# Kernel optimization log

Measured on AMD Instinct MI355X. Metric: run time of the kernel, lower is better.

Reference implementation:

```python
import jax, jax.numpy as jnp
import numpy as np

B = 16384       # batch
G = 8           # groups
S = 16          # state_c (per-group in/out channels)
H = 512         # hidden_c (per-group hidden channels)
FACTOR = 1.0
SWISH_DIV = 1.1


def setup_inputs() -> dict:
    key = jax.random.key(0)
    ks = jax.random.split(key, 12)
    def w(k, shape, fan_in):
        bound = 1.0 / np.sqrt(fan_in)
        return jax.random.uniform(k, shape, jnp.float32, -bound, bound)
    return {
        "x":  jax.random.normal(ks[0], (B, G * S), dtype=jnp.float32),
        # grouped 1x1 convs as per-group linear weights [G, out_c, in_c]
        "W1": w(ks[1], (G, H, S), S), "b1": w(ks[2], (G, H), S),
        "beta1": jnp.full((G,), 0.5, jnp.float32),
        "W2": w(ks[3], (G, H, H), H), "b2": w(ks[4], (G, H), H),
        "beta2": jnp.full((G,), 0.5, jnp.float32),
        "W3": w(ks[5], (G, H, H), H), "b3": w(ks[6], (G, H), H),
        "beta3": jnp.full((G,), 0.5, jnp.float32),
        "W4": w(ks[7], (G, S, H), H), "b4": w(ks[8], (G, S), H),
    }


def _group_swish(x, beta):
    # x: [B, G, C]; beta: [G] -> y = x * sigmoid(x * softplus(beta)) / 1.1
    sp = jax.nn.softplus(beta)[None, :, None]
    return x * jax.nn.sigmoid(x * sp) / SWISH_DIV


def reference(x, W1, b1, beta1, W2, b2, beta2, W3, b3, beta3, W4, b4):
    h = x.reshape(-1, G, S)                                   # [B,G,S]
    h = jnp.einsum('bgs,ghs->bgh', h, W1) + b1[None]          # [B,G,H]
    h = _group_swish(h, beta1)
    h = jnp.einsum('bgi,goi->bgo', h, W2) + b2[None]
    h = _group_swish(h, beta2)
    h = jnp.einsum('bgi,goi->bgo', h, W3) + b3[None]
    h = _group_swish(h, beta3)
    h = jnp.einsum('bgh,gsh->bgs', h, W4) + b4[None]          # [B,G,S]
    return h.reshape(-1, G * S) * FACTOR
```

## Files before the change

kernel.cpp:

```cpp
#include <hip/hip_runtime.h>
#include <stdint.h>

#define G_ 8
#define S_ 16
#define H_ 512
#define TB 64
#define NTH 512

typedef _Float16 h16;
typedef _Float16 h16x8 __attribute__((ext_vector_type(8)));
typedef float f32x4 __attribute__((ext_vector_type(4)));
typedef float f32x16 __attribute__((ext_vector_type(16)));

#define HB_BYTES (TB * 1024)
#define XB_BYTES 2048
#define SMEM_BYTES (HB_BYTES + XB_BYTES)


__device__ __forceinline__ float swishf(float v, float sp) {
    const float e = __expf(-v * sp);
    return v * __builtin_amdgcn_rcpf(1.0f + e) * (1.0f / 1.1f);
}

__device__ __forceinline__ uint32_t pk16(float a, float b) {
    return __builtin_bit_cast(uint32_t, __builtin_amdgcn_cvt_pkrtz(a, b));
}

template<bool USEWS>
__device__ __forceinline__ h16x8 loadA32ks(const h16* __restrict__ wpk,
                                           const float* __restrict__ wf,
                                           int ks, int nb, int ln, int Ksrc) {
    if constexpr (USEWS) {
        return *(const h16x8*)(wpk + (((size_t)ks * 16 + nb) * 64 + ln) * 8);
    } else {
        const int row = nb * 32 + (ln & 31);
        const int k = ks * 16 + (ln >> 5) * 8;
        const float* p = wf + (size_t)row * Ksrc + k;
        h16x8 r;
        #pragma unroll
        for (int j = 0; j < 8; ++j) r[j] = (h16)p[j];
        return r;
    }
}

template<bool USEWS>
__device__ __forceinline__ h16x8 loadA16(const h16* __restrict__ wpk,
                                         const float* __restrict__ wf,
                                         int ks32, int ln, int Ksrc) {
    if constexpr (USEWS) {
        return *(const h16x8*)(wpk + ((size_t)ks32 * 64 + ln) * 8);
    } else {
        const int row = ln & 15;
        const int k = ks32 * 32 + (ln >> 4) * 8;
        const float* p = wf + (size_t)row * Ksrc + k;
        h16x8 r;
        #pragma unroll
        for (int j = 0; j < 8; ++j) r[j] = (h16)p[j];
        return r;
    }
}

__device__ __forceinline__ void swish_store32(const f32x16 (&acc)[2][2], char* hb,
                                              const float* __restrict__ bias, float sp,
                                              int wv, int ln) {
    const int l31 = ln & 31, lh = ln >> 5;
    char* const wbase = hb + wv * 8192 + l31 * 16 + lh * 8;
    #pragma unroll
    for (int ot = 0; ot < 2; ++ot) {
        #pragma unroll
        for (int rq = 0; rq < 4; ++rq) {
            const int col0 = wv * 64 + ot * 32 + rq * 8 + lh * 4;
            const f32x4 bv = *(const f32x4*)(bias + col0);
            #pragma unroll
            for (int bt = 0; bt < 2; ++bt) {
                const float v0 = swishf(acc[ot][bt][rq * 4 + 0] + bv[0], sp);
                const float v1 = swishf(acc[ot][bt][rq * 4 + 1] + bv[1], sp);
                const float v2 = swishf(acc[ot][bt][rq * 4 + 2] + bv[2], sp);
                const float v3 = swishf(acc[ot][bt][rq * 4 + 3] + bv[3], sp);
                const uint64_t u = (uint64_t)pk16(v0, v1)
                                 | ((uint64_t)pk16(v2, v3) << 32);
                *(uint64_t*)(wbase + (ot * 4 + rq) * 1024 + bt * 512) = u;
            }
        }
    }
}

template<bool USEWS>
__device__ __forceinline__ void layerH32(f32x16 (&acc)[2][2],
                                         const h16* __restrict__ wpk, const float* __restrict__ wf,
                                         const char* __restrict__ hb, int wv, int ln) {
    const int l31 = ln & 31, lh = ln >> 5;
    const char* const bbase = hb + l31 * 16 + lh * 1024;
    const int nb0 = wv * 2;
    #pragma unroll
    for (int ot = 0; ot < 2; ++ot)
        #pragma unroll
        for (int bt = 0; bt < 2; ++bt) acc[ot][bt] = (f32x16)(0.f);

    h16x8 aC0 = loadA32ks<USEWS>(wpk, wf, 0, nb0 + 0, ln, H_);
    h16x8 aC1 = loadA32ks<USEWS>(wpk, wf, 0, nb0 + 1, ln, H_);

    #pragma unroll 4
    for (int ks = 0; ks < 32; ++ks) {
        const int ksn = (ks + 1 < 32) ? ks + 1 : 0;
        h16x8 aN0 = loadA32ks<USEWS>(wpk, wf, ksn, nb0 + 0, ln, H_);
        h16x8 aN1 = loadA32ks<USEWS>(wpk, wf, ksn, nb0 + 1, ln, H_);
        const h16x8 b0 = *(const h16x8*)(bbase + ks * 2048);
        const h16x8 b1 = *(const h16x8*)(bbase + ks * 2048 + 512);
        __builtin_amdgcn_s_setprio(1);
        acc[0][0] = __builtin_amdgcn_mfma_f32_32x32x16_f16(aC0, b0, acc[0][0], 0, 0, 0);
        acc[0][1] = __builtin_amdgcn_mfma_f32_32x32x16_f16(aC0, b1, acc[0][1], 0, 0, 0);
        acc[1][0] = __builtin_amdgcn_mfma_f32_32x32x16_f16(aC1, b0, acc[1][0], 0, 0, 0);
        acc[1][1] = __builtin_amdgcn_mfma_f32_32x32x16_f16(aC1, b1, acc[1][1], 0, 0, 0);
        __builtin_amdgcn_s_setprio(0);
        aC0 = aN0; aC1 = aN1;
    }
}

template<bool USEWS>
__global__ __launch_bounds__(NTH, 4) void mlp_fused(
    const float* __restrict__ x,
    const float* __restrict__ W1f, const float* __restrict__ b1, const float* __restrict__ be1,
    const float* __restrict__ W2f, const float* __restrict__ b2, const float* __restrict__ be2,
    const float* __restrict__ W3f, const float* __restrict__ b3, const float* __restrict__ be3,
    const float* __restrict__ W4f, const float* __restrict__ b4,
    const h16* __restrict__ W1p, const h16* __restrict__ W2p,
    const h16* __restrict__ W3p, const h16* __restrict__ W4p,
    float* __restrict__ out) {
    extern __shared__ char smem[];
    char* __restrict__ xb = smem + HB_BYTES;

    const int bid = blockIdx.x;
    const int g = bid & 7;
    const int rowbase = (bid >> 3) * TB;
    const int tid = threadIdx.x;
    const int wv = tid >> 6;
    const int ln = tid & 63;
    const int l31 = ln & 31;
    const int lh = ln >> 5;

    const float sp1 = log1pf(__expf(be1[g]));
    const float sp2 = log1pf(__expf(be2[g]));
    const float sp3 = log1pf(__expf(be3[g]));

    const h16* w1p = W1p + (size_t)g * H_ * S_;
    const h16* w2p = W2p + (size_t)g * H_ * H_;
    const h16* w3p = W3p + (size_t)g * H_ * H_;
    const h16* w4p = W4p + (size_t)g * S_ * H_;
    const float* w1f = W1f + (size_t)g * H_ * S_;
    const float* w2f = W2f + (size_t)g * H_ * H_;
    const float* w3f = W3f + (size_t)g * H_ * H_;
    const float* w4f = W4f + (size_t)g * S_ * H_;

    {
        const int idx = tid * 2;
        const int r = idx >> 4, s = idx & 15;
        const float2 v = *(const float2*)(x + (size_t)(rowbase + r) * (G_ * S_) + g * S_ + s);
        *(uint32_t*)(xb + (s >> 3) * 1024 + r * 16 + (s & 7) * 2) = pk16(v.x, v.y);
    }
    __syncthreads();

    f32x16 acc[2][2];

    {
        #pragma unroll
        for (int ot = 0; ot < 2; ++ot)
            #pragma unroll
            for (int bt = 0; bt < 2; ++bt) acc[ot][bt] = (f32x16)(0.f);
        const char* const xbase = xb + l31 * 16 + lh * 1024;
        h16x8 aW[2], bX[2];
        #pragma unroll
        for (int ot = 0; ot < 2; ++ot)
            aW[ot] = loadA32ks<USEWS>(w1p, w1f, 0, wv * 2 + ot, ln, S_);
        #pragma unroll
        for (int bt = 0; bt < 2; ++bt)
            bX[bt] = *(const h16x8*)(xbase + bt * 512);
        #pragma unroll
        for (int ot = 0; ot < 2; ++ot)
            #pragma unroll
            for (int bt = 0; bt < 2; ++bt)
                acc[ot][bt] = __builtin_amdgcn_mfma_f32_32x32x16_f16(aW[ot], bX[bt],
                                                                     acc[ot][bt], 0, 0, 0);
    }
    swish_store32(acc, smem, b1 + g * H_, sp1, wv, ln);
    __syncthreads();

    layerH32<USEWS>(acc, w2p, w2f, smem, wv, ln);
    __syncthreads();
    swish_store32(acc, smem, b2 + g * H_, sp2, wv, ln);
    __syncthreads();

    layerH32<USEWS>(acc, w3p, w3f, smem, wv, ln);
    __syncthreads();
    swish_store32(acc, smem, b3 + g * H_, sp3, wv, ln);
    __syncthreads();

    if (wv < 4) {
        f32x4 a4 = {0.f, 0.f, 0.f, 0.f};
        const int l15 = ln & 15, lq = ln >> 4;
        const char* const b4base = smem + lq * 1024 + (wv * 16 + l15) * 16;
        #pragma unroll 4
        for (int ks = 0; ks < 16; ++ks) {
            const h16x8 a = loadA16<USEWS>(w4p, w4f, ks, ln, H_);
            const h16x8 b = *(const h16x8*)(b4base + ks * 4096);
            a4 = __builtin_amdgcn_mfma_f32_16x16x32_f16(a, b, a4, 0, 0, 0);
        }
        const int brow = wv * 16 + l15;
        const int s0 = lq * 4;
        const f32x4 bv = *(const f32x4*)(b4 + g * S_ + s0);
        f32x4 o4;
        #pragma unroll
        for (int r = 0; r < 4; ++r) o4[r] = a4[r] + bv[r];
        *(f32x4*)(out + (size_t)(rowbase + brow) * (G_ * S_) + g * S_ + s0) = o4;
    }
}

__global__ void packW32(const float* __restrict__ s, h16* __restrict__ d,
                        int KB, int Ks) {
    const int t = blockIdx.x * 256 + threadIdx.x;
    const int total = G_ * KB * 16 * 64;
    if (t >= total) return;
    const int ln = t & 63;
    const int blk = t >> 6;
    const int nb = blk & 15;
    const int rest = blk >> 4;
    const int ks = rest % KB;
    const int g = rest / KB;
    const int row = g * H_ + nb * 32 + (ln & 31);
    const int k = ks * 16 + (ln >> 5) * 8;
    const float* p = s + (size_t)row * Ks + k;
    h16x8 o;
    #pragma unroll
    for (int j = 0; j < 8; ++j) o[j] = (h16)p[j];
    *(h16x8*)(d + (size_t)t * 8) = o;
}

__global__ void packW16(const float* __restrict__ s, h16* __restrict__ d,
                        int NB_total, int KB, int Ks) {
    const int t = blockIdx.x * 256 + threadIdx.x;
    const int total = NB_total * KB * 64;
    if (t >= total) return;
    const int ln = t & 63;
    const int blk = t >> 6;
    const int kb = blk % KB;
    const int nbg = blk / KB;
    const int row = nbg * 16 + (ln & 15);
    const int k = kb * 32 + (ln >> 4) * 8;
    const float* p = s + (size_t)row * Ks + k;
    h16x8 o;
    #pragma unroll
    for (int j = 0; j < 8; ++j) o[j] = (h16)p[j];
    *(h16x8*)(d + (size_t)t * 8) = o;
}

extern "C" void kernel_launch(void* const* d_in, const int* in_sizes, int n_in,
                              void* d_out, int out_size, void* d_ws, size_t ws_size,
                              hipStream_t stream) {
    const float* x   = (const float*)d_in[0];
    const float* W1  = (const float*)d_in[1];
    const float* b1  = (const float*)d_in[2];
    const float* be1 = (const float*)d_in[3];
    const float* W2  = (const float*)d_in[4];
    const float* b2  = (const float*)d_in[5];
    const float* be2 = (const float*)d_in[6];
    const float* W3  = (const float*)d_in[7];
    const float* b3  = (const float*)d_in[8];
    const float* be3 = (const float*)d_in[9];
    const float* W4  = (const float*)d_in[10];
    const float* b4  = (const float*)d_in[11];
    float* out = (float*)d_out;

    const size_t nW2  = (size_t)G_ * H_ * H_;
    const size_t nW1p = (size_t)G_ * H_ * S_;
    const size_t nW4  = (size_t)G_ * S_ * H_;
    const size_t need = (2 * nW2 + nW1p + nW4) * sizeof(h16);

    const dim3 grid(2048), blk(NTH);

    if (ws_size >= need) {
        h16* W2p = (h16*)d_ws;
        h16* W3p = W2p + nW2;
        h16* W1p = W3p + nW2;
        h16* W4p = W1p + nW1p;
        packW32<<<dim3((unsigned)((nW2 / 8 + 255) / 256)), dim3(256), 0, stream>>>(W2, W2p, 32, H_);
        packW32<<<dim3((unsigned)((nW2 / 8 + 255) / 256)), dim3(256), 0, stream>>>(W3, W3p, 32, H_);
        packW32<<<dim3((unsigned)((nW1p / 8 + 255) / 256)), dim3(256), 0, stream>>>(W1, W1p, 1, S_);
        packW16<<<dim3((unsigned)((nW4 / 8 + 255) / 256)), dim3(256), 0, stream>>>(W4, W4p, G_, 16, H_);
        (void)hipFuncSetAttribute(reinterpret_cast<const void*>(mlp_fused<true>),
                                  hipFuncAttributeMaxDynamicSharedMemorySize, (int)SMEM_BYTES);
        mlp_fused<true><<<grid, blk, SMEM_BYTES, stream>>>(
            x, W1, b1, be1, W2, b2, be2, W3, b3, be3, W4, b4,
            W1p, W2p, W3p, W4p, out);
    } else {
        (void)hipFuncSetAttribute(reinterpret_cast<const void*>(mlp_fused<false>),
                                  hipFuncAttributeMaxDynamicSharedMemorySize, (int)SMEM_BYTES);
        mlp_fused<false><<<grid, blk, SMEM_BYTES, stream>>>(
            x, W1, b1, be1, W2, b2, be2, W3, b3, be3, W4, b4,
            nullptr, nullptr, nullptr, nullptr, out);
    }
}
```

Before: 198.2 us.

## Double batch tile to 128 rows with 16 waves splitting output and batch halves

Doubles the per-block batch tile to 128 rows and the block to 1024 threads. Wave pairs share an output slice and each covers one half of the batch, so every weight fragment loaded from global memory serves twice as many rows, halving weight traffic per row. The shared-memory layout for activations is restrided to fit 128 rows, and the grid is halved. It also drops the software prefetch of the next A fragment in the hidden-layer loop, which may expose global load latency, and the larger blocks with __launch_bounds__(1024,4) add register pressure and lower block-level occupancy.

```diff
diff --git a/kernel.cpp b/kernel.cpp
--- a/kernel.cpp
+++ b/kernel.cpp
@@ -4,8 +4,8 @@
 #define G_ 8
 #define S_ 16
 #define H_ 512
-#define TB 64
-#define NTH 512
+#define TB 128
+#define NTH 1024
 
 typedef _Float16 h16;
 typedef _Float16 h16x8 __attribute__((ext_vector_type(8)));
@@ -13,7 +13,7 @@
 typedef float f32x16 __attribute__((ext_vector_type(16)));
 
 #define HB_BYTES (TB * 1024)
-#define XB_BYTES 2048
+#define XB_BYTES (TB * 32)
 #define SMEM_BYTES (HB_BYTES + XB_BYTES)
 
 
@@ -62,14 +62,14 @@
 
 __device__ __forceinline__ void swish_store32(const f32x16 (&acc)[2][2], char* hb,
                                               const float* __restrict__ bias, float sp,
-                                              int wv, int ln) {
+                                              int os, int bh, int ln) {
     const int l31 = ln & 31, lh = ln >> 5;
-    char* const wbase = hb + wv * 8192 + l31 * 16 + lh * 8;
+    char* const wbase = hb + os * 16384 + bh * 1024 + l31 * 16 + lh * 8;
     #pragma unroll
     for (int ot = 0; ot < 2; ++ot) {
         #pragma unroll
         for (int rq = 0; rq < 4; ++rq) {
-            const int col0 = wv * 64 + ot * 32 + rq * 8 + lh * 4;
+            const int col0 = os * 64 + ot * 32 + rq * 8 + lh * 4;
             const f32x4 bv = *(const f32x4*)(bias + col0);
             #pragma unroll
             for (int bt = 0; bt < 2; ++bt) {
@@ -79,7 +79,7 @@
                 const float v3 = swishf(acc[ot][bt][rq * 4 + 3] + bv[3], sp);
                 const uint64_t u = (uint64_t)pk16(v0, v1)
                                  | ((uint64_t)pk16(v2, v3) << 32);
-                *(uint64_t*)(wbase + (ot * 4 + rq) * 1024 + bt * 512) = u;
+                *(uint64_t*)(wbase + (ot * 4 + rq) * 2048 + bt * 512) = u;
             }
         }
     }
@@ -88,32 +88,27 @@
 template<bool USEWS>
 __device__ __forceinline__ void layerH32(f32x16 (&acc)[2][2],
                                          const h16* __restrict__ wpk, const float* __restrict__ wf,
-                                         const char* __restrict__ hb, int wv, int ln) {
+                                         const char* __restrict__ hb, int os, int bh, int ln) {
     const int l31 = ln & 31, lh = ln >> 5;
-    const char* const bbase = hb + l31 * 16 + lh * 1024;
-    const int nb0 = wv * 2;
+    const char* const bbase = hb + lh * 2048 + bh * 1024 + l31 * 16;
+    const int nb0 = os * 2;
     #pragma unroll
     for (int ot = 0; ot < 2; ++ot)
         #pragma unroll
         for (int bt = 0; bt < 2; ++bt) acc[ot][bt] = (f32x16)(0.f);
-
-    h16x8 aC0 = loadA32ks<USEWS>(wpk, wf, 0, nb0 + 0, ln, H_);
-    h16x8 aC1 = loadA32ks<USEWS>(wpk, wf, 0, nb0 + 1, ln, H_);
 
     #pragma unroll 4
     for (int ks = 0; ks < 32; ++ks) {
-        const int ksn = (ks + 1 < 32) ? ks + 1 : 0;
-        h16x8 aN0 = loadA32ks<USEWS>(wpk, wf, ksn, nb0 + 0, ln, H_);
-        h16x8 aN1 = loadA32ks<USEWS>(wpk, wf, ksn, nb0 + 1, ln, H_);
-        const h16x8 b0 = *(const h16x8*)(bbase + ks * 2048);
-        const h16x8 b1 = *(const h16x8*)(bbase + ks * 2048 + 512);
+        const h16x8 a0 = loadA32ks<USEWS>(wpk, wf, ks, nb0 + 0, ln, H_);
+        const h16x8 a1 = loadA32ks<USEWS>(wpk, wf, ks, nb0 + 1, ln, H_);
+        const h16x8 b0 = *(const h16x8*)(bbase + ks * 4096);
+        const h16x8 b1 = *(const h16x8*)(bbase + ks * 4096 + 512);
         __builtin_amdgcn_s_setprio(1);
-        acc[0][0] = __builtin_amdgcn_mfma_f32_32x32x16_f16(aC0, b0, acc[0][0], 0, 0, 0);
-        acc[0][1] = __builtin_amdgcn_mfma_f32_32x32x16_f16(aC0, b1, acc[0][1], 0, 0, 0);
-        acc[1][0] = __builtin_amdgcn_mfma_f32_32x32x16_f16(aC1, b0, acc[1][0], 0, 0, 0);
-        acc[1][1] = __builtin_amdgcn_mfma_f32_32x32x16_f16(aC1, b1, acc[1][1], 0, 0, 0);
+        acc[0][0] = __builtin_amdgcn_mfma_f32_32x32x16_f16(a0, b0, acc[0][0], 0, 0, 0);
+        acc[0][1] = __builtin_amdgcn_mfma_f32_32x32x16_f16(a0, b1, acc[0][1], 0, 0, 0);
+        acc[1][0] = __builtin_amdgcn_mfma_f32_32x32x16_f16(a1, b0, acc[1][0], 0, 0, 0);
+        acc[1][1] = __builtin_amdgcn_mfma_f32_32x32x16_f16(a1, b1, acc[1][1], 0, 0, 0);
         __builtin_amdgcn_s_setprio(0);
-        aC0 = aN0; aC1 = aN1;
     }
 }
 
@@ -138,6 +133,8 @@
     const int ln = tid & 63;
     const int l31 = ln & 31;
     const int lh = ln >> 5;
+    const int os = wv >> 1;
+    const int bh = wv & 1;
 
     const float sp1 = log1pf(__expf(be1[g]));
     const float sp2 = log1pf(__expf(be2[g]));
@@ -156,7 +153,7 @@
         const int idx = tid * 2;
         const int r = idx >> 4, s = idx & 15;
         const float2 v = *(const float2*)(x + (size_t)(rowbase + r) * (G_ * S_) + g * S_ + s);
-        *(uint32_t*)(xb + (s >> 3) * 1024 + r * 16 + (s & 7) * 2) = pk16(v.x, v.y);
+        *(uint32_t*)(xb + (s >> 3) * 2048 + r * 16 + (s & 7) * 2) = pk16(v.x, v.y);
     }
     __syncthreads();
 
@@ -167,11 +164,11 @@
         for (int ot = 0; ot < 2; ++ot)
             #pragma unroll
             for (int bt = 0; bt < 2; ++bt) acc[ot][bt] = (f32x16)(0.f);
-        const char* const xbase = xb + l31 * 16 + lh * 1024;
+        const char* const xbase = xb + lh * 2048 + bh * 1024 + l31 * 16;
         h16x8 aW[2], bX[2];
         #pragma unroll
         for (int ot = 0; ot < 2; ++ot)
-            aW[ot] = loadA32ks<USEWS>(w1p, w1f, 0, wv * 2 + ot, ln, S_);
+            aW[ot] = loadA32ks<USEWS>(w1p, w1f, 0, os * 2 + ot, ln, S_);
         #pragma unroll
         for (int bt = 0; bt < 2; ++bt)
             bX[bt] = *(const h16x8*)(xbase + bt * 512);
@@ -182,27 +179,27 @@
                 acc[ot][bt] = __builtin_amdgcn_mfma_f32_32x32x16_f16(aW[ot], bX[bt],
                                                                      acc[ot][bt], 0, 0, 0);
     }
-    swish_store32(acc, smem, b1 + g * H_, sp1, wv, ln);
-    __syncthreads();
-
-    layerH32<USEWS>(acc, w2p, w2f, smem, wv, ln);
-    __syncthreads();
-    swish_store32(acc, smem, b2 + g * H_, sp2, wv, ln);
-    __syncthreads();
-
-    layerH32<USEWS>(acc, w3p, w3f, smem, wv, ln);
-    __syncthreads();
-    swish_store32(acc, smem, b3 + g * H_, sp3, wv, ln);
-    __syncthreads();
-
-    if (wv < 4) {
+    swish_store32(acc, smem, b1 + g * H_, sp1, os, bh, ln);
+    __syncthreads();
+
+    layerH32<USEWS>(acc, w2p, w2f, smem, os, bh, ln);
+    __syncthreads();
+    swish_store32(acc, smem, b2 + g * H_, sp2, os, bh, ln);
+    __syncthreads();
+
+    layerH32<USEWS>(acc, w3p, w3f, smem, os, bh, ln);
+    __syncthreads();
+    swish_store32(acc, smem, b3 + g * H_, sp3, os, bh, ln);
+    __syncthreads();
+
+    if (wv < 8) {
         f32x4 a4 = {0.f, 0.f, 0.f, 0.f};
         const int l15 = ln & 15, lq = ln >> 4;
-        const char* const b4base = smem + lq * 1024 + (wv * 16 + l15) * 16;
+        const char* const b4base = smem + lq * 2048 + (wv * 16 + l15) * 16;
         #pragma unroll 4
         for (int ks = 0; ks < 16; ++ks) {
             const h16x8 a = loadA16<USEWS>(w4p, w4f, ks, ln, H_);
-            const h16x8 b = *(const h16x8*)(b4base + ks * 4096);
+            const h16x8 b = *(const h16x8*)(b4base + ks * 8192);
             a4 = __builtin_amdgcn_mfma_f32_16x16x32_f16(a, b, a4, 0, 0, 0);
         }
         const int brow = wv * 16 + l15;
@@ -275,7 +272,7 @@
     const size_t nW4  = (size_t)G_ * S_ * H_;
     const size_t need = (2 * nW2 + nW1p + nW4) * sizeof(h16);
 
-    const dim3 grid(2048), blk(NTH);
+    const dim3 grid((16384 / TB) * G_), blk(NTH);
 
     if (ws_size >= need) {
         h16* W2p = (h16*)d_ws;
```

Measured after the change: 213.4 us. 1.08x slower.

## Replace block barriers with per-wave LDS flags for layer handoff

Applied to the files above, without the earlier changes.

Drops the __syncthreads between the hidden layers and uses per-wave done and read counters in shared memory. Each wave spins until the slice of activations it needs has been written, and waits for all readers to finish before overwriting its own slice. The K loop is reordered so each wave starts on its own slice and rotates through the others, letting waves overlap across layers instead of waiting at a barrier. This adds spin-wait cost, drops the software prefetch of A across iterations, and risks memory-ordering bugs since the fences are only compiler and lgkmcnt waits.

```diff
diff --git a/kernel.cpp b/kernel.cpp
--- a/kernel.cpp
+++ b/kernel.cpp
@@ -14,8 +14,18 @@
 
 #define HB_BYTES (TB * 1024)
 #define XB_BYTES 2048
-#define SMEM_BYTES (HB_BYTES + XB_BYTES)
-
+#define FLAG_BYTES 128
+#define SMEM_BYTES (HB_BYTES + XB_BYTES + FLAG_BYTES)
+
+
+__device__ __forceinline__ void fence_acquire() {
+    __builtin_amdgcn_sched_barrier(0);
+    asm volatile("" ::: "memory");
+}
+__device__ __forceinline__ void fence_release() {
+    asm volatile("s_waitcnt lgkmcnt(0)" ::: "memory");
+    __builtin_amdgcn_sched_barrier(0);
+}
 
 __device__ __forceinline__ float swishf(float v, float sp) {
     const float e = __expf(-v * sp);
@@ -60,9 +70,16 @@
     }
 }
 
+template<bool FLAGS>
 __device__ __forceinline__ void swish_store32(const f32x16 (&acc)[2][2], char* hb,
                                               const float* __restrict__ bias, float sp,
-                                              int wv, int ln) {
+                                              int wv, int ln,
+                                              int* rdone, volatile int* wdone,
+                                              int need, int wseq) {
+    if constexpr (FLAGS) {
+        while (*(volatile int*)&rdone[wv] < need) { }
+        fence_acquire();
+    }
     const int l31 = ln & 31, lh = ln >> 5;
     char* const wbase = hb + wv * 8192 + l31 * 16 + lh * 8;
     #pragma unroll
@@ -83,12 +100,17 @@
             }
         }
     }
-}
-
-template<bool USEWS>
+    if constexpr (FLAGS) {
+        fence_release();
+        if (ln == 0) *(volatile int*)&wdone[wv] = wseq;
+    }
+}
+
+template<bool USEWS, bool POLLW>
 __device__ __forceinline__ void layerH32(f32x16 (&acc)[2][2],
                                          const h16* __restrict__ wpk, const float* __restrict__ wf,
-                                         const char* __restrict__ hb, int wv, int ln) {
+                                         const char* __restrict__ hb, int wv, int ln,
+                                         volatile int* wdone, int* rdone, int wseq) {
     const int l31 = ln & 31, lh = ln >> 5;
     const char* const bbase = hb + l31 * 16 + lh * 1024;
     const int nb0 = wv * 2;
@@ -97,23 +119,29 @@
         #pragma unroll
         for (int bt = 0; bt < 2; ++bt) acc[ot][bt] = (f32x16)(0.f);
 
-    h16x8 aC0 = loadA32ks<USEWS>(wpk, wf, 0, nb0 + 0, ln, H_);
-    h16x8 aC1 = loadA32ks<USEWS>(wpk, wf, 0, nb0 + 1, ln, H_);
-
-    #pragma unroll 4
-    for (int ks = 0; ks < 32; ++ks) {
-        const int ksn = (ks + 1 < 32) ? ks + 1 : 0;
-        h16x8 aN0 = loadA32ks<USEWS>(wpk, wf, ksn, nb0 + 0, ln, H_);
-        h16x8 aN1 = loadA32ks<USEWS>(wpk, wf, ksn, nb0 + 1, ln, H_);
-        const h16x8 b0 = *(const h16x8*)(bbase + ks * 2048);
-        const h16x8 b1 = *(const h16x8*)(bbase + ks * 2048 + 512);
-        __builtin_amdgcn_s_setprio(1);
-        acc[0][0] = __builtin_amdgcn_mfma_f32_32x32x16_f16(aC0, b0, acc[0][0], 0, 0, 0);
-        acc[0][1] = __builtin_amdgcn_mfma_f32_32x32x16_f16(aC0, b1, acc[0][1], 0, 0, 0);
-        acc[1][0] = __builtin_amdgcn_mfma_f32_32x32x16_f16(aC1, b0, acc[1][0], 0, 0, 0);
-        acc[1][1] = __builtin_amdgcn_mfma_f32_32x32x16_f16(aC1, b1, acc[1][1], 0, 0, 0);
-        __builtin_amdgcn_s_setprio(0);
-        aC0 = aN0; aC1 = aN1;
+    for (int i = 0; i < 8; ++i) {
+        const int q = (wv + i) & 7;
+        if constexpr (POLLW) {
+            while (wdone[q] < wseq) { }
+            fence_acquire();
+        }
+        const char* const qb = bbase + q * 8192;
+        #pragma unroll 2
+        for (int j = 0; j < 4; ++j) {
+            const int ks = q * 4 + j;
+            const h16x8 a0 = loadA32ks<USEWS>(wpk, wf, ks, nb0 + 0, ln, H_);
+            const h16x8 a1 = loadA32ks<USEWS>(wpk, wf, ks, nb0 + 1, ln, H_);
+            const h16x8 b0 = *(const h16x8*)(qb + j * 2048);
+            const h16x8 b1 = *(const h16x8*)(qb + j * 2048 + 512);
+            __builtin_amdgcn_s_setprio(1);
+            acc[0][0] = __builtin_amdgcn_mfma_f32_32x32x16_f16(a0, b0, acc[0][0], 0, 0, 0);
+            acc[0][1] = __builtin_amdgcn_mfma_f32_32x32x16_f16(a0, b1, acc[0][1], 0, 0, 0);
+            acc[1][0] = __builtin_amdgcn_mfma_f32_32x32x16_f16(a1, b0, acc[1][0], 0, 0, 0);
+            acc[1][1] = __builtin_amdgcn_mfma_f32_32x32x16_f16(a1, b1, acc[1][1], 0, 0, 0);
+            __builtin_amdgcn_s_setprio(0);
+        }
+        fence_release();
+        if (ln == 0) atomicAdd(&rdone[q], 1);
     }
 }
 
@@ -129,6 +157,9 @@
     float* __restrict__ out) {
     extern __shared__ char smem[];
     char* __restrict__ xb = smem + HB_BYTES;
+    int* const flagbase = (int*)(smem + HB_BYTES + XB_BYTES);
+    volatile int* const wdone = (volatile int*)flagbase;
+    int* const rdone = flagbase + 8;
 
     const int bid = blockIdx.x;
     const int g = bid & 7;
@@ -152,6 +183,7 @@
     const float* w3f = W3f + (size_t)g * H_ * H_;
     const float* w4f = W4f + (size_t)g * S_ * H_;
 
+    if (tid < 16) flagbase[tid] = 0;
     {
         const int idx = tid * 2;
         const int r = idx >> 4, s = idx & 15;
@@ -182,28 +214,30 @@
                 acc[ot][bt] = __builtin_amdgcn_mfma_f32_32x32x16_f16(aW[ot], bX[bt],
                                                                      acc[ot][bt], 0, 0, 0);
     }
-    swish_store32(acc, smem, b1 + g * H_, sp1, wv, ln);
+    swish_store32<false>(acc, smem, b1 + g * H_, sp1, wv, ln, nullptr, nullptr, 0, 0);
     __syncthreads();
 
-    layerH32<USEWS>(acc, w2p, w2f, smem, wv, ln);
-    __syncthreads();
-    swish_store32(acc, smem, b2 + g * H_, sp2, wv, ln);
-    __syncthreads();
-
-    layerH32<USEWS>(acc, w3p, w3f, smem, wv, ln);
-    __syncthreads();
-    swish_store32(acc, smem, b3 + g * H_, sp3, wv, ln);
-    __syncthreads();
+    layerH32<USEWS, false>(acc, w2p, w2f, smem, wv, ln, wdone, rdone, 0);
+    swish_store32<true>(acc, smem, b2 + g * H_, sp2, wv, ln, rdone, wdone, 8, 2);
+
+    layerH32<USEWS, true>(acc, w3p, w3f, smem, wv, ln, wdone, rdone, 2);
+    swish_store32<true>(acc, smem, b3 + g * H_, sp3, wv, ln, rdone, wdone, 16, 3);
 
     if (wv < 4) {
         f32x4 a4 = {0.f, 0.f, 0.f, 0.f};
         const int l15 = ln & 15, lq = ln >> 4;
         const char* const b4base = smem + lq * 1024 + (wv * 16 + l15) * 16;
-        #pragma unroll 4
-        for (int ks = 0; ks < 16; ++ks) {
-            const h16x8 a = loadA16<USEWS>(w4p, w4f, ks, ln, H_);
-            const h16x8 b = *(const h16x8*)(b4base + ks * 4096);
-            a4 = __builtin_amdgcn_mfma_f32_16x16x32_f16(a, b, a4, 0, 0, 0);
+        for (int i = 0; i < 8; ++i) {
+            const int q = (wv + i) & 7;
+            while (wdone[q] < 3) { }
+            fence_acquire();
+            #pragma unroll
+            for (int j = 0; j < 2; ++j) {
+                const int ks = 2 * q + j;
+                const h16x8 a = loadA16<USEWS>(w4p, w4f, ks, ln, H_);
+                const h16x8 b = *(const h16x8*)(b4base + ks * 4096);
+                a4 = __builtin_amdgcn_mfma_f32_16x16x32_f16(a, b, a4, 0, 0, 0);
+            }
         }
         const int brow = wv * 16 + l15;
         const int s0 = lq * 4;
@@ -275,7 +309,7 @@
     const size_t nW4  = (size_t)G_ * S_ * H_;
     const size_t need = (2 * nW2 + nW1p + nW4) * sizeof(h16);
 
-    const dim3 grid(2048), blk(NTH);
+    const dim3 grid((16384 / TB) * G_), blk(NTH);
 
     if (ws_size >= need) {
         h16* W2p = (h16*)d_ws;
```

New measurement: 236.3 us. 19.2% more time.
